# Optimization experiments

Hardware: AMD Instinct MI355X
Metric: run time of the kernel (lower is better)

The kernel has to match this reference:

```python
import jax, jax.numpy as jnp
import numpy as np

EARTH_RADIUS = 6371.0
TAU = 75.0
EPS = 1e-9


def setup_inputs() -> dict:
    key = jax.random.key(0)
    k1, k2, k3 = jax.random.split(key, 3)
    B, C = 512, 32768
    pred_logits = jax.random.normal(k1, (B, C), dtype=jnp.float32)
    # lat in [-90, 90], lon in [-180, 180]
    u_true = jax.random.uniform(k2, (B, 2), dtype=jnp.float32)
    latlon = u_true * jnp.array([180.0, 360.0], jnp.float32) - jnp.array([90.0, 180.0], jnp.float32)
    u_geo = jax.random.uniform(k3, (C, 2), dtype=jnp.float32)
    geocell_coords = u_geo * jnp.array([180.0, 360.0], jnp.float32) - jnp.array([90.0, 180.0], jnp.float32)
    return {"pred_logits": pred_logits, "latlon": latlon, "geocell_coords": geocell_coords}


def _haversine_matrix(latlon, geocell_coords):
    # latlon: [B,2] degrees, geocell_coords: [C,2] degrees -> [B,C] km
    t = jnp.deg2rad(latlon)          # [B,2]
    g = jnp.deg2rad(geocell_coords)  # [C,2]
    lat1 = t[:, 0:1]                 # [B,1]
    lon1 = t[:, 1:2]
    lat2 = g[None, :, 0]             # [1,C]
    lon2 = g[None, :, 1]
    dlat = lat2 - lat1               # [B,C]
    dlon = lon2 - lon1
    a = jnp.sin(dlat * 0.5) ** 2 + jnp.cos(lat1) * jnp.cos(lat2) * jnp.sin(dlon * 0.5) ** 2
    return 2.0 * EARTH_RADIUS * jnp.arcsin(jnp.sqrt(a))


def reference(pred_logits, latlon, geocell_coords):
    dist = _haversine_matrix(latlon, geocell_coords)          # [B,C]
    target = jnp.exp(-dist / TAU)                              # [B,C]
    target = target / jnp.sum(target, axis=1, keepdims=True)
    pred_probs = jax.nn.softmax(pred_logits, axis=1)
    loss = jnp.mean(jnp.sum(-target * jnp.log(pred_probs + EPS), axis=1))
    return loss
```

## Files before the change

kernel.cpp:

```cpp
#include <hip/hip_runtime.h>
#include <math.h>

#define PI_F 3.14159265358979323846f

__global__ void geo_precompute(const float* __restrict__ geo,
                               float4* __restrict__ tab, int C) {
    int c = blockIdx.x * blockDim.x + threadIdx.x;
    if (c >= C) return;
    float lat = geo[2 * c + 0];
    float lon = geo[2 * c + 1];
    float hl = lat * (PI_F / 360.0f);
    float ho = lon * (PI_F / 360.0f);
    float sa, ca, so, co;
    __sincosf(hl, &sa, &ca);
    __sincosf(ho, &so, &co);
    tab[c] = make_float4(sa, ca, so, co);
}

__device__ __forceinline__ float asin01(float x) {
    float p = -0.0012624911f;
    p = fmaf(p, x, 0.0066700901f);
    p = fmaf(p, x, -0.0170881256f);
    p = fmaf(p, x, 0.0308918810f);
    p = fmaf(p, x, -0.0501743046f);
    p = fmaf(p, x, 0.0889789874f);
    p = fmaf(p, x, -0.2145988016f);
    p = fmaf(p, x, 1.5707963050f);
    float s = sqrtf(fmaxf(1.0f - x, 0.0f));
    return fmaf(-s, p, 1.57079632679f);
}

__global__ __launch_bounds__(1024) void loss_kernel(
    const float* __restrict__ logits, const float* __restrict__ latlon,
    const float4* __restrict__ tab, float* __restrict__ out,
    int C, float inv_B) {
    const int b = blockIdx.x;
    const int tid = threadIdx.x;

    float hlat1 = latlon[2 * b + 0] * (PI_F / 360.0f);
    float hlon1 = latlon[2 * b + 1] * (PI_F / 360.0f);
    float s1a, c1a, s1o, c1o;
    __sincosf(hlat1, &s1a, &c1a);
    __sincosf(hlon1, &s1o, &c1o);
    float cl1 = c1a * c1a - s1a * s1a;

    const float4* lp = (const float4*)(logits + (size_t)b * C);
    const int n4 = C >> 2;

    float Z = 0.0f, S0 = 0.0f, S1 = 0.0f;

    for (int i = tid; i < n4; i += blockDim.x) {
        float4 l4 = lp[i];
        float4 g0 = tab[4 * i + 0];
        float4 g1 = tab[4 * i + 1];
        float4 g2 = tab[4 * i + 2];
        float4 g3 = tab[4 * i + 3];
        float lv[4] = {l4.x, l4.y, l4.z, l4.w};
        float4 gv[4] = {g0, g1, g2, g3};
#pragma unroll
        for (int j = 0; j < 4; j++) {
            float sa = gv[j].x, ca = gv[j].y, so = gv[j].z, co = gv[j].w;
            float sdlat = fmaf(sa, c1a, -ca * s1a);
            float sdlon = fmaf(so, c1o, -co * s1o);
            float cl2 = fmaf(ca, ca, -sa * sa);
            float a = fmaf(sdlat, sdlat, (cl1 * cl2) * (sdlon * sdlon));
            float x = fminf(sqrtf(fmaxf(a, 0.0f)), 1.0f);
            float dist = (2.0f * 6371.0f) * asin01(x);
            float w = __expf(dist * (-1.0f / 75.0f));
            float l = lv[j];
            Z += __expf(l);
            S0 += w;
            S1 = fmaf(w, l, S1);
        }
    }

    for (int off = 32; off > 0; off >>= 1) {
        Z += __shfl_down(Z, off);
        S0 += __shfl_down(S0, off);
        S1 += __shfl_down(S1, off);
    }
    __shared__ float sZ[16], sS0[16], sS1[16];
    const int wave = tid >> 6, lane = tid & 63;
    if (lane == 0) { sZ[wave] = Z; sS0[wave] = S0; sS1[wave] = S1; }
    __syncthreads();
    if (tid < 64) {
        Z = (tid < 16) ? sZ[tid] : 0.0f;
        S0 = (tid < 16) ? sS0[tid] : 0.0f;
        S1 = (tid < 16) ? sS1[tid] : 0.0f;
        for (int off = 8; off > 0; off >>= 1) {
            Z += __shfl_down(Z, off);
            S0 += __shfl_down(S0, off);
            S1 += __shfl_down(S1, off);
        }
        if (tid == 0) {
            float loss_b = logf(Z) - S1 / S0;
            atomicAdd(out, loss_b * inv_B);
        }
    }
}

extern "C" void kernel_launch(void* const* d_in, const int* in_sizes, int n_in,
                              void* d_out, int out_size, void* d_ws, size_t ws_size,
                              hipStream_t stream) {
    const float* logits = (const float*)d_in[0];
    const float* latlon = (const float*)d_in[1];
    const float* geo    = (const float*)d_in[2];
    float* out = (float*)d_out;

    const int B = in_sizes[1] / 2;
    const int C = in_sizes[2] / 2;
    float4* tab = (float4*)d_ws;

    hipMemsetAsync(out, 0, sizeof(float) * out_size, stream);
    geo_precompute<<<(C + 255) / 256, 256, 0, stream>>>(geo, tab, C);
    loss_kernel<<<B, 1024, 0, stream>>>(logits, latlon, tab, out, C, 1.0f / (float)B);
}
```

Before: 122.1 us.

## Use unit-vector dot product for haversine and cheaper asin polynomial

Precomputes 3D unit vectors for each geocell, so each pair's haversine term becomes a dot product: a = (1 - dot)/2. It replaces the 8-term asin polynomial with a 4-term one, folds the distance scale and the exp constant into one fma, and uses raw hardware sqrt. It also drops the separate memset launch by zeroing the output inside the precompute kernel. The goal is less ALU work per pair and one fewer launch, at the cost of lower asin accuracy. The dot-product form can also lose precision for nearby points.

```diff
diff --git a/kernel.cpp b/kernel.cpp
--- a/kernel.cpp
+++ b/kernel.cpp
@@ -4,30 +4,36 @@
 #define PI_F 3.14159265358979323846f
 
 __global__ void geo_precompute(const float* __restrict__ geo,
-                               float4* __restrict__ tab, int C) {
+                               float4* __restrict__ tab, int C,
+                               float* __restrict__ out) {
     int c = blockIdx.x * blockDim.x + threadIdx.x;
+    if (c == 0) out[0] = 0.0f;
     if (c >= C) return;
-    float lat = geo[2 * c + 0];
-    float lon = geo[2 * c + 1];
-    float hl = lat * (PI_F / 360.0f);
-    float ho = lon * (PI_F / 360.0f);
-    float sa, ca, so, co;
-    __sincosf(hl, &sa, &ca);
-    __sincosf(ho, &so, &co);
-    tab[c] = make_float4(sa, ca, so, co);
+    float lat = geo[2 * c + 0] * (PI_F / 180.0f);
+    float lon = geo[2 * c + 1] * (PI_F / 180.0f);
+    float sla, cla, slo, clo;
+    __sincosf(lat, &sla, &cla);
+    __sincosf(lon, &slo, &clo);
+    tab[c] = make_float4(cla * clo, cla * slo, sla, 0.0f);
 }
 
-__device__ __forceinline__ float asin01(float x) {
-    float p = -0.0012624911f;
-    p = fmaf(p, x, 0.0066700901f);
-    p = fmaf(p, x, -0.0170881256f);
-    p = fmaf(p, x, 0.0308918810f);
-    p = fmaf(p, x, -0.0501743046f);
-    p = fmaf(p, x, 0.0889789874f);
-    p = fmaf(p, x, -0.2145988016f);
-    p = fmaf(p, x, 1.5707963050f);
-    float s = sqrtf(fmaxf(1.0f - x, 0.0f));
-    return fmaf(-s, p, 1.57079632679f);
+__device__ __forceinline__ void pair_accum(float l, float4 g,
+                                           float v1x, float v1y, float v1z,
+                                           float& Z, float& S0, float& S1) {
+    float dot = fmaf(g.x, v1x, fmaf(g.y, v1y, g.z * v1z));
+    float a = fmaf(dot, -0.5f, 0.5f);
+    a = fmaxf(a, 0.0f);
+    float x = __builtin_amdgcn_sqrtf(a);
+    float omx = fmaxf(1.0f - x, 0.0f);
+    float s = __builtin_amdgcn_sqrtf(omx);
+    float p = fmaf(fmaf(fmaf(-0.0187293f, x, 0.0742610f), x, -0.2121144f),
+                   x, 1.5707288f);
+    float wexp = fmaf(169.8933333f, s * p, -266.867824f);
+    float w = __expf(wexp);
+    float ez = __expf(l);
+    Z += ez;
+    S0 += w;
+    S1 = fmaf(w, l, S1);
 }
 
 __global__ __launch_bounds__(1024) void loss_kernel(
@@ -37,41 +43,26 @@
     const int b = blockIdx.x;
     const int tid = threadIdx.x;
 
-    float hlat1 = latlon[2 * b + 0] * (PI_F / 360.0f);
-    float hlon1 = latlon[2 * b + 1] * (PI_F / 360.0f);
-    float s1a, c1a, s1o, c1o;
-    __sincosf(hlat1, &s1a, &c1a);
-    __sincosf(hlon1, &s1o, &c1o);
-    float cl1 = c1a * c1a - s1a * s1a;
+    float lat = latlon[2 * b + 0] * (PI_F / 180.0f);
+    float lon = latlon[2 * b + 1] * (PI_F / 180.0f);
+    float sla, cla, slo, clo;
+    __sincosf(lat, &sla, &cla);
+    __sincosf(lon, &slo, &clo);
+    const float v1x = cla * clo, v1y = cla * slo, v1z = sla;
 
     const float4* lp = (const float4*)(logits + (size_t)b * C);
     const int n4 = C >> 2;
 
     float Z = 0.0f, S0 = 0.0f, S1 = 0.0f;
 
-    for (int i = tid; i < n4; i += blockDim.x) {
+    for (int i = tid; i < n4; i += 1024) {
         float4 l4 = lp[i];
-        float4 g0 = tab[4 * i + 0];
-        float4 g1 = tab[4 * i + 1];
-        float4 g2 = tab[4 * i + 2];
-        float4 g3 = tab[4 * i + 3];
-        float lv[4] = {l4.x, l4.y, l4.z, l4.w};
-        float4 gv[4] = {g0, g1, g2, g3};
-#pragma unroll
-        for (int j = 0; j < 4; j++) {
-            float sa = gv[j].x, ca = gv[j].y, so = gv[j].z, co = gv[j].w;
-            float sdlat = fmaf(sa, c1a, -ca * s1a);
-            float sdlon = fmaf(so, c1o, -co * s1o);
-            float cl2 = fmaf(ca, ca, -sa * sa);
-            float a = fmaf(sdlat, sdlat, (cl1 * cl2) * (sdlon * sdlon));
-            float x = fminf(sqrtf(fmaxf(a, 0.0f)), 1.0f);
-            float dist = (2.0f * 6371.0f) * asin01(x);
-            float w = __expf(dist * (-1.0f / 75.0f));
-            float l = lv[j];
-            Z += __expf(l);
-            S0 += w;
-            S1 = fmaf(w, l, S1);
-        }
+        const float4* t = tab + 4 * i;
+        float4 t0 = t[0], t1 = t[1], t2 = t[2], t3 = t[3];
+        pair_accum(l4.x, t0, v1x, v1y, v1z, Z, S0, S1);
+        pair_accum(l4.y, t1, v1x, v1y, v1z, Z, S0, S1);
+        pair_accum(l4.z, t2, v1x, v1y, v1z, Z, S0, S1);
+        pair_accum(l4.w, t3, v1x, v1y, v1z, Z, S0, S1);
     }
 
     for (int off = 32; off > 0; off >>= 1) {
@@ -111,7 +102,6 @@
     const int C = in_sizes[2] / 2;
     float4* tab = (float4*)d_ws;
 
-    hipMemsetAsync(out, 0, sizeof(float) * out_size, stream);
-    geo_precompute<<<(C + 255) / 256, 256, 0, stream>>>(geo, tab, C);
+    geo_precompute<<<(C + 255) / 256, 256, 0, stream>>>(geo, tab, C, out);
     loss_kernel<<<B, 1024, 0, stream>>>(logits, latlon, tab, out, C, 1.0f / (float)B);
 }
```

Result: faster. 111.4 us (-8.8%).
